# Optimization experiments

Measured on AMD Instinct MI355X. Metric: run time of the kernel, lower is better.

The kernel has to match this reference:

```python
import jax, jax.numpy as jnp
import numpy as np

B, N, IN_F = 8, 1024, 512
H, D = 4, 128  # num_heads, out_features; H*D == IN_F for residual
LN_EPS = 1e-5
NEG_INF = -1e9


def setup_inputs() -> dict:
    key = jax.random.key(0)
    ks = jax.random.split(key, 7)
    x = jax.random.normal(ks[0], (B, N, IN_F), dtype=jnp.float32)
    mask = jax.random.randint(ks[1], (B, N), 0, 2, dtype=jnp.int32)
    # xavier-uniform-ish init scales
    W = jax.random.uniform(ks[2], (IN_F, H * D), dtype=jnp.float32, minval=-1.0, maxval=1.0) * (1.414 * np.sqrt(6.0 / (IN_F + H * D)))
    a_src = jax.random.uniform(ks[3], (H, D), dtype=jnp.float32, minval=-1.0, maxval=1.0) * (1.414 * np.sqrt(6.0 / (H + D)))
    a_dst = jax.random.uniform(ks[4], (H, D), dtype=jnp.float32, minval=-1.0, maxval=1.0) * (1.414 * np.sqrt(6.0 / (H + D)))
    gamma = jnp.ones((H * D,), dtype=jnp.float32)
    beta = jnp.zeros((H * D,), dtype=jnp.float32)
    return {"x": x, "mask": mask, "W": W, "a_src": a_src, "a_dst": a_dst, "gamma": gamma, "beta": beta}


def _layernorm(y, gamma, beta):
    mu = jnp.mean(y, axis=-1, keepdims=True)
    var = jnp.var(y, axis=-1, keepdims=True)
    return (y - mu) * jax.lax.rsqrt(var + LN_EPS) * gamma + beta


def reference(x, mask, W, a_src, a_dst, gamma, beta):
    b, n, _ = x.shape
    h = (x @ W).reshape(b, n, H, D)                      # [B,N,H,D]
    e_i = jnp.einsum('bnhd,hd->bnh', h, a_src)           # [B,N,H]
    e_j = jnp.einsum('bnhd,hd->bnh', h, a_dst)           # [B,N,H]
    e = jax.nn.leaky_relu(e_i[:, :, None, :] + e_j[:, None, :, :], 0.2)  # [B,N,N,H]
    mm = mask[:, None, :, None] * mask[:, :, None, None]  # [B,N,N,1]
    e = jnp.where(mm == 0, NEG_INF, e)
    attn = jax.nn.softmax(e, axis=2)                     # softmax over neighbors j
    h_prime = jnp.einsum('bnjh,bjhd->bnhd', attn, h).reshape(b, n, H * D)
    return _layernorm(h_prime + x, gamma, beta)
```

## Files before the change

kernel.cpp:

```cpp
#include <hip/hip_runtime.h>
#include <math.h>

#define Bsz 8
#define Nn 1024
#define Ff 512
#define Hh 4
#define Dd 128

typedef float f32x4 __attribute__((ext_vector_type(4)));
typedef short bf16x8 __attribute__((ext_vector_type(8)));

__device__ inline uint f2b1(float a) {
    union { float f; uint u; } v; v.f = a;
    return (v.u + 0x7fffu + ((v.u >> 16) & 1u)) >> 16;
}
__device__ inline uint f2b_pk(float a, float b) { return f2b1(a) | (f2b1(b) << 16); }


__global__ __launch_bounds__(256) void conv_xw(const float* __restrict__ X,
                                               const float* __restrict__ Wm,
                                               ushort* __restrict__ Xc,
                                               ushort* __restrict__ Wc) {
    __shared__ float tile[8 * 520];
    const int bi = blockIdx.x, tid = threadIdx.x;
    if (bi < 512) {
        const int mtile = bi, kblk = tid >> 2, m15b = (tid & 3) * 4;
        #pragma unroll
        for (int c = 0; c < 4; ++c) {
            int m15 = m15b + c;
            const float4* xp = (const float4*)(X + (size_t)(mtile * 16 + m15) * Ff + kblk * 8);
            float4 f0 = xp[0], f1 = xp[1];
            uint4 o = { f2b_pk(f0.x, f0.y), f2b_pk(f0.z, f0.w),
                        f2b_pk(f1.x, f1.y), f2b_pk(f1.z, f1.w) };
            *(uint4*)(Xc + (((size_t)(mtile * 64 + kblk) * 16 + m15) << 3)) = o;
        }
    } else {
        const int kb = bi - 512;
        const int l = tid & 63, wv = tid >> 6;
        const int col0 = l * 8;
        #pragma unroll
        for (int rsel = 0; rsel < 2; ++rsel) {
            int kr = wv + rsel * 4;
            const float4* wp = (const float4*)(Wm + (size_t)(kb * 8 + kr) * Ff + col0);
            float4 a = wp[0], c = wp[1];
            *(float4*)(&tile[kr * 520 + col0]) = a;
            *(float4*)(&tile[kr * 520 + col0 + 4]) = c;
        }
        __syncthreads();
        #pragma unroll
        for (int rsel = 0; rsel < 2; ++rsel) {
            int n = tid + rsel * 256;
            float v[8];
            #pragma unroll
            for (int u = 0; u < 8; ++u) v[u] = tile[u * 520 + n];
            uint4 o = { f2b_pk(v[0], v[1]), f2b_pk(v[2], v[3]),
                        f2b_pk(v[4], v[5]), f2b_pk(v[6], v[7]) };
            int nc = n >> 7, nt = (n >> 4) & 7, n15 = n & 15;
            *(uint4*)(Wc + ((size_t)(((nc * 64 + kb) * 8 + nt) * 16 + n15) << 3)) = o;
        }
    }
}

__global__ __launch_bounds__(256, 4) void gemm_xw(const ushort* __restrict__ Xc,
                                                  const ushort* __restrict__ Wc,
                                                  const float* __restrict__ a_src,
                                                  const float* __restrict__ a_dst,
                                                  ushort* __restrict__ hT,
                                                  float* __restrict__ ei,
                                                  float* __restrict__ ej) {
    const int idx = blockIdx.x;
    const int b = idx & 7, sub = idx >> 3;
    const int mi = sub & 15, nc = sub >> 4;
    const int tid = threadIdx.x;
    const int w = tid >> 6, lane = tid & 63, quad = lane >> 4, l16 = lane & 15;
    const int mtile = (b * 16 + mi) * 4 + w;

    f32x4 z = {0.f, 0.f, 0.f, 0.f};
    f32x4 acc[8];
    #pragma unroll
    for (int nt = 0; nt < 8; ++nt) acc[nt] = z;

    const ushort* ap = Xc + ((size_t)mtile << 13) + quad * 128 + l16 * 8;
    const ushort* bp = Wc + ((size_t)nc << 16) + quad * 1024 + l16 * 8;

    bf16x8 ac = *(const bf16x8*)(ap);
    bf16x8 bc[8];
    #pragma unroll
    for (int nt = 0; nt < 8; ++nt) bc[nt] = *(const bf16x8*)(bp + nt * 128);

    #pragma unroll 2
    for (int s = 0; s < 16; ++s) {
        bf16x8 an, bn[8];
        if (s < 15) {
            an = *(const bf16x8*)(ap + (s + 1) * 512);
            #pragma unroll
            for (int nt = 0; nt < 8; ++nt)
                bn[nt] = *(const bf16x8*)(bp + (s + 1) * 4096 + nt * 128);
        }
        #pragma unroll
        for (int nt = 0; nt < 8; ++nt)
            acc[nt] = __builtin_amdgcn_mfma_f32_16x16x32_bf16(ac, bc[nt], acc[nt], 0, 0, 0);
        if (s < 15) {
            ac = an;
            #pragma unroll
            for (int nt = 0; nt < 8; ++nt) bc[nt] = bn[nt];
        }
    }

    const int nseq = (mi * 4 + w) * 16 + quad * 4;
    const int jb = nseq >> 5, js = nseq & 31;
    #pragma unroll
    for (int nt = 0; nt < 8; ++nt) {
        uint2 pv;
        pv.x = f2b_pk(acc[nt][0], acc[nt][1]);
        pv.y = f2b_pk(acc[nt][2], acc[nt][3]);
        int hd = nc * 128 + nt * 16 + l16;
        *(uint2*)(hT + ((size_t)(b * 32 + jb)) * 16384 + (size_t)hd * 32 + js) = pv;
    }

    {
        float as4[8], ad4[8];
        #pragma unroll
        for (int nt = 0; nt < 8; ++nt) {
            as4[nt] = a_src[nc * 128 + nt * 16 + l16];
            ad4[nt] = a_dst[nc * 128 + nt * 16 + l16];
        }
        #pragma unroll
        for (int rr = 0; rr < 4; ++rr) {
            float v1 = 0.f, v2 = 0.f;
            #pragma unroll
            for (int nt = 0; nt < 8; ++nt) {
                v1 += acc[nt][rr] * as4[nt];
                v2 += acc[nt][rr] * ad4[nt];
            }
            #pragma unroll
            for (int off = 1; off < 16; off <<= 1) {
                v1 += __shfl_xor(v1, off);
                v2 += __shfl_xor(v2, off);
            }
            if (l16 == 0) {
                int n = nseq + rr;
                ei[((b * 4 + nc) << 10) + n] = v1;
                ej[((b * 4 + nc) << 10) + n] = v2;
            }
        }
    }
}

__global__ __launch_bounds__(512, 2) void attn_pv(const ushort* __restrict__ hT,
                                                  const float* __restrict__ ei_g,
                                                  const float* __restrict__ ej_g,
                                                  const int* __restrict__ mask,
                                                  const float* __restrict__ X,
                                                  const float* __restrict__ gamma,
                                                  const float* __restrict__ beta,
                                                  float* __restrict__ out) {
    __shared__ float s_ep[32 * 516];
    __shared__ float s_as[4][32];

    const int idx = blockIdx.x;
    const int b = idx & 7, i0 = (idx >> 3) * 32;
    const int tid = threadIdx.x;
    const int w = tid >> 6, w4 = w & 3, jh = w >> 2;
    const int lane = tid & 63, quad = lane >> 4, l16 = lane & 15;

    const float* ejh = ej_g + ((b * 4 + w4) << 10);
    const int* mkb = mask + (b << 10);

    float maxej = -3.0e38f;
    #pragma unroll
    for (int k = 0; k < 16; ++k) maxej = fmaxf(maxej, ejh[lane + 64 * k]);
    #pragma unroll
    for (int off = 1; off < 64; off <<= 1) maxej = fmaxf(maxej, __shfl_xor(maxej, off));

    const float ei0 = ei_g[((b * 4 + w4) << 10) + i0 + l16];
    const float ei1 = ei_g[((b * 4 + w4) << 10) + i0 + 16 + l16];
    const int mi0 = mkb[i0 + l16];
    const int mi1 = mkb[i0 + 16 + l16];
    float m0, m1;
    { float t = ei0 + maxej; m0 = mi0 ? fmaxf(t, 0.2f * t) : -1e9f; }
    { float t = ei1 + maxej; m1 = mi1 ? fmaxf(t, 0.2f * t) : -1e9f; }

    f32x4 z = {0.f, 0.f, 0.f, 0.f};
    f32x4 acc[2][8], asum[2];
    #pragma unroll
    for (int it = 0; it < 2; ++it) { asum[it] = z;
        #pragma unroll
        for (int dt = 0; dt < 8; ++dt) acc[it][dt] = z; }
    bf16x8 ones;
    #pragma unroll
    for (int q = 0; q < 8; ++q) ones[q] = (short)0x3F80;

    const ushort* hTb = hT + ((size_t)(b * 32)) * 16384 + (size_t)(w4 * 128) * 32
                        + l16 * 32 + quad * 8;

    bf16x8 cur[8];
    {
        const ushort* h0 = hTb + (size_t)(jh * 16) * 16384;
        #pragma unroll
        for (int dt = 0; dt < 8; ++dt) cur[dt] = *(const bf16x8*)(h0 + dt * 512);
    }

    #pragma unroll 2
    for (int r = 0; r < 16; ++r) {
        bf16x8 nxt[8];
        if (r < 15) {
            const ushort* hn = hTb + (size_t)(jh * 16 + r + 1) * 16384;
            #pragma unroll
            for (int dt = 0; dt < 8; ++dt) nxt[dt] = *(const bf16x8*)(hn + dt * 512);
        }
        const int jq = (jh * 16 + r) * 32 + quad * 8;
        float4 e0 = *(const float4*)(ejh + jq);
        float4 e1 = *(const float4*)(ejh + jq + 4);
        int4 q0 = *(const int4*)(mkb + jq);
        int4 q1 = *(const int4*)(mkb + jq + 4);
        float ev[8] = {e0.x, e0.y, e0.z, e0.w, e1.x, e1.y, e1.z, e1.w};
        int   mv[8] = {q0.x, q0.y, q0.z, q0.w, q1.x, q1.y, q1.z, q1.w};
        float wv0[8], wv1[8];
        #pragma unroll
        for (int u = 0; u < 8; ++u) {
            float t0 = ei0 + ev[u];
            float l0 = fmaxf(t0, 0.2f * t0);
            wv0[u] = __expf(((mi0 && mv[u]) ? l0 : -1e9f) - m0);
            float t1 = ei1 + ev[u];
            float l1 = fmaxf(t1, 0.2f * t1);
            wv1[u] = __expf(((mi1 && mv[u]) ? l1 : -1e9f) - m1);
        }
        union { uint4 u; bf16x8 v; } af0, af1;
        af0.u.x = f2b_pk(wv0[0], wv0[1]); af0.u.y = f2b_pk(wv0[2], wv0[3]);
        af0.u.z = f2b_pk(wv0[4], wv0[5]); af0.u.w = f2b_pk(wv0[6], wv0[7]);
        af1.u.x = f2b_pk(wv1[0], wv1[1]); af1.u.y = f2b_pk(wv1[2], wv1[3]);
        af1.u.z = f2b_pk(wv1[4], wv1[5]); af1.u.w = f2b_pk(wv1[6], wv1[7]);
        asum[0] = __builtin_amdgcn_mfma_f32_16x16x32_bf16(af0.v, ones, asum[0], 0, 0, 0);
        asum[1] = __builtin_amdgcn_mfma_f32_16x16x32_bf16(af1.v, ones, asum[1], 0, 0, 0);
        #pragma unroll
        for (int dt = 0; dt < 8; ++dt) {
            acc[0][dt] = __builtin_amdgcn_mfma_f32_16x16x32_bf16(af0.v, cur[dt], acc[0][dt], 0, 0, 0);
            acc[1][dt] = __builtin_amdgcn_mfma_f32_16x16x32_bf16(af1.v, cur[dt], acc[1][dt], 0, 0, 0);
        }
        if (r < 15) {
            #pragma unroll
            for (int dt = 0; dt < 8; ++dt) cur[dt] = nxt[dt];
        }
    }

    if (jh == 1) {
        #pragma unroll
        for (int it = 0; it < 2; ++it)
            #pragma unroll
            for (int dt = 0; dt < 8; ++dt)
                #pragma unroll
                for (int rr = 0; rr < 4; ++rr)
                    s_ep[(it * 16 + quad * 4 + rr) * 516 + w4 * 128 + dt * 16 + l16] =
                        acc[it][dt][rr];
        if (l16 == 0) {
            #pragma unroll
            for (int it = 0; it < 2; ++it)
                #pragma unroll
                for (int rr = 0; rr < 4; ++rr)
                    s_as[w4][it * 16 + quad * 4 + rr] = asum[it][rr];
        }
    }
    __syncthreads();
    if (jh == 0) {
        float rs[2][4];
        #pragma unroll
        for (int it = 0; it < 2; ++it)
            #pragma unroll
            for (int rr = 0; rr < 4; ++rr)
                rs[it][rr] = 1.f / (asum[it][rr] + s_as[w4][it * 16 + quad * 4 + rr]);
        #pragma unroll
        for (int it = 0; it < 2; ++it)
            #pragma unroll
            for (int dt = 0; dt < 8; ++dt)
                #pragma unroll
                for (int rr = 0; rr < 4; ++rr) {
                    int off = (it * 16 + quad * 4 + rr) * 516 + w4 * 128 + dt * 16 + l16;
                    s_ep[off] = (acc[it][dt][rr] + s_ep[off]) * rs[it][rr];
                }
    }
    __syncthreads();

    #pragma unroll
    for (int q = 0; q < 4; ++q) {
        int ir = w * 4 + q;
        int ig = i0 + ir;
        float4 p0 = *(const float4*)(&s_ep[ir * 516 + lane * 8]);
        float4 p1 = *(const float4*)(&s_ep[ir * 516 + lane * 8 + 4]);
        const float* xp = X + (((size_t)((b << 10) + ig)) << 9) + lane * 8;
        float4 x0 = *(const float4*)(xp);
        float4 x1 = *(const float4*)(xp + 4);
        float v[8] = {p0.x + x0.x, p0.y + x0.y, p0.z + x0.z, p0.w + x0.w,
                      p1.x + x1.x, p1.y + x1.y, p1.z + x1.z, p1.w + x1.w};
        float s1 = 0.f, s2 = 0.f;
        #pragma unroll
        for (int u = 0; u < 8; ++u) { s1 += v[u]; s2 += v[u] * v[u]; }
        #pragma unroll
        for (int off = 1; off < 64; off <<= 1) { s1 += __shfl_xor(s1, off); s2 += __shfl_xor(s2, off); }
        float mean = s1 * (1.f / 512.f);
        float var  = s2 * (1.f / 512.f) - mean * mean;
        float rstd = rsqrtf(var + 1e-5f);
        int f0i = lane * 8;
        float4 g0 = *(const float4*)(gamma + f0i);
        float4 g1 = *(const float4*)(gamma + f0i + 4);
        float4 be0 = *(const float4*)(beta + f0i);
        float4 be1 = *(const float4*)(beta + f0i + 4);
        float* op = out + (((size_t)((b << 10) + ig)) << 9) + f0i;
        float4 o0, o1;
        o0.x = (v[0] - mean) * rstd * g0.x + be0.x;
        o0.y = (v[1] - mean) * rstd * g0.y + be0.y;
        o0.z = (v[2] - mean) * rstd * g0.z + be0.z;
        o0.w = (v[3] - mean) * rstd * g0.w + be0.w;
        o1.x = (v[4] - mean) * rstd * g1.x + be1.x;
        o1.y = (v[5] - mean) * rstd * g1.y + be1.y;
        o1.z = (v[6] - mean) * rstd * g1.z + be1.z;
        o1.w = (v[7] - mean) * rstd * g1.w + be1.w;
        *(float4*)op = o0;
        *(float4*)(op + 4) = o1;
    }
}

extern "C" void kernel_launch(void* const* d_in, const int* in_sizes, int n_in,
                              void* d_out, int out_size, void* d_ws, size_t ws_size,
                              hipStream_t stream) {
    const float* x     = (const float*)d_in[0];
    const int*   mask  = (const int*)d_in[1];
    const float* W     = (const float*)d_in[2];
    const float* a_src = (const float*)d_in[3];
    const float* a_dst = (const float*)d_in[4];
    const float* gamma = (const float*)d_in[5];
    const float* beta  = (const float*)d_in[6];
    float* out = (float*)d_out;

    ushort* hT = (ushort*)d_ws;
    ushort* Xc = hT + (size_t)8 * 512 * 1024;
    ushort* Wc = Xc + (size_t)8 * 1024 * 512;
    float* ei = (float*)(Wc + (size_t)512 * 512);
    float* ej = ei + 32768;

    conv_xw<<<dim3(576), 256, 0, stream>>>(x, W, Xc, Wc);
    gemm_xw<<<dim3(512), 256, 0, stream>>>(Xc, Wc, a_src, a_dst, hT, ei, ej);
    attn_pv<<<dim3(256), 512, 0, stream>>>(hT, ei, ej, mask, x, gamma, beta, out);
}
```

Measured before the change: 131.9 us.

## Deepen register prefetch to two stages in GEMM and attention loops, remap conv tiles

Both the XW GEMM and the attention-aggregation loop now keep two register buffers of operand fragments and load two steps ahead, replacing the one-step prefetch with its register copy. This is meant to hide more global-load latency behind the MFMA work. To make room for the extra registers, the GEMM's launch-bounds minimum occupancy drops from 4 to 2 blocks, which risks hiding less latency through occupancy. The conversion kernel also remaps its block index to m-tiles in an interleaved order, which changes the memory access pattern across blocks.

```diff
diff --git a/kernel.cpp b/kernel.cpp
--- a/kernel.cpp
+++ b/kernel.cpp
@@ -24,7 +24,8 @@
     __shared__ float tile[8 * 520];
     const int bi = blockIdx.x, tid = threadIdx.x;
     if (bi < 512) {
-        const int mtile = bi, kblk = tid >> 2, m15b = (tid & 3) * 4;
+        const int mtile = (bi & 7) * 64 + (bi >> 3);
+        const int kblk = tid >> 2, m15b = (tid & 3) * 4;
         #pragma unroll
         for (int c = 0; c < 4; ++c) {
             int m15 = m15b + c;
@@ -61,7 +62,7 @@
     }
 }
 
-__global__ __launch_bounds__(256, 4) void gemm_xw(const ushort* __restrict__ Xc,
+__global__ __launch_bounds__(256, 2) void gemm_xw(const ushort* __restrict__ Xc,
                                                   const ushort* __restrict__ Wc,
                                                   const float* __restrict__ a_src,
                                                   const float* __restrict__ a_dst,
@@ -83,27 +84,27 @@
     const ushort* ap = Xc + ((size_t)mtile << 13) + quad * 128 + l16 * 8;
     const ushort* bp = Wc + ((size_t)nc << 16) + quad * 1024 + l16 * 8;
 
-    bf16x8 ac = *(const bf16x8*)(ap);
-    bf16x8 bc[8];
-    #pragma unroll
-    for (int nt = 0; nt < 8; ++nt) bc[nt] = *(const bf16x8*)(bp + nt * 128);
+    bf16x8 ab[2];
+    bf16x8 bb[2][8];
+    ab[0] = *(const bf16x8*)(ap);
+    ab[1] = *(const bf16x8*)(ap + 512);
+    #pragma unroll
+    for (int nt = 0; nt < 8; ++nt) {
+        bb[0][nt] = *(const bf16x8*)(bp + nt * 128);
+        bb[1][nt] = *(const bf16x8*)(bp + 4096 + nt * 128);
+    }
 
     #pragma unroll 2
     for (int s = 0; s < 16; ++s) {
-        bf16x8 an, bn[8];
-        if (s < 15) {
-            an = *(const bf16x8*)(ap + (s + 1) * 512);
+        const int c = s & 1;
+        #pragma unroll
+        for (int nt = 0; nt < 8; ++nt)
+            acc[nt] = __builtin_amdgcn_mfma_f32_16x16x32_bf16(ab[c], bb[c][nt], acc[nt], 0, 0, 0);
+        if (s + 2 < 16) {
+            ab[c] = *(const bf16x8*)(ap + (s + 2) * 512);
             #pragma unroll
             for (int nt = 0; nt < 8; ++nt)
-                bn[nt] = *(const bf16x8*)(bp + (s + 1) * 4096 + nt * 128);
-        }
-        #pragma unroll
-        for (int nt = 0; nt < 8; ++nt)
-            acc[nt] = __builtin_amdgcn_mfma_f32_16x16x32_bf16(ac, bc[nt], acc[nt], 0, 0, 0);
-        if (s < 15) {
-            ac = an;
-            #pragma unroll
-            for (int nt = 0; nt < 8; ++nt) bc[nt] = bn[nt];
+                bb[c][nt] = *(const bf16x8*)(bp + (s + 2) * 4096 + nt * 128);
         }
     }
 
@@ -194,21 +195,17 @@
     const ushort* hTb = hT + ((size_t)(b * 32)) * 16384 + (size_t)(w4 * 128) * 32
                         + l16 * 32 + quad * 8;
 
-    bf16x8 cur[8];
-    {
-        const ushort* h0 = hTb + (size_t)(jh * 16) * 16384;
-        #pragma unroll
-        for (int dt = 0; dt < 8; ++dt) cur[dt] = *(const bf16x8*)(h0 + dt * 512);
+    bf16x8 B[2][8];
+    #pragma unroll
+    for (int c = 0; c < 2; ++c) {
+        const ushort* h0 = hTb + (size_t)(jh * 16 + c) * 16384;
+        #pragma unroll
+        for (int dt = 0; dt < 8; ++dt) B[c][dt] = *(const bf16x8*)(h0 + dt * 512);
     }
 
     #pragma unroll 2
     for (int r = 0; r < 16; ++r) {
-        bf16x8 nxt[8];
-        if (r < 15) {
-            const ushort* hn = hTb + (size_t)(jh * 16 + r + 1) * 16384;
-            #pragma unroll
-            for (int dt = 0; dt < 8; ++dt) nxt[dt] = *(const bf16x8*)(hn + dt * 512);
-        }
+        const int c = r & 1;
         const int jq = (jh * 16 + r) * 32 + quad * 8;
         float4 e0 = *(const float4*)(ejh + jq);
         float4 e1 = *(const float4*)(ejh + jq + 4);
@@ -235,12 +232,13 @@
         asum[1] = __builtin_amdgcn_mfma_f32_16x16x32_bf16(af1.v, ones, asum[1], 0, 0, 0);
         #pragma unroll
         for (int dt = 0; dt < 8; ++dt) {
-            acc[0][dt] = __builtin_amdgcn_mfma_f32_16x16x32_bf16(af0.v, cur[dt], acc[0][dt], 0, 0, 0);
-            acc[1][dt] = __builtin_amdgcn_mfma_f32_16x16x32_bf16(af1.v, cur[dt], acc[1][dt], 0, 0, 0);
-        }
-        if (r < 15) {
-            #pragma unroll
-            for (int dt = 0; dt < 8; ++dt) cur[dt] = nxt[dt];
+            acc[0][dt] = __builtin_amdgcn_mfma_f32_16x16x32_bf16(af0.v, B[c][dt], acc[0][dt], 0, 0, 0);
+            acc[1][dt] = __builtin_amdgcn_mfma_f32_16x16x32_bf16(af1.v, B[c][dt], acc[1][dt], 0, 0, 0);
+        }
+        if (r + 2 < 16) {
+            const ushort* hn = hTb + (size_t)(jh * 16 + r + 2) * 16384;
+            #pragma unroll
+            for (int dt = 0; dt < 8; ++dt) B[c][dt] = *(const bf16x8*)(hn + dt * 512);
         }
     }
 
```

New measurement: 125.9 us. 4.6% less time.
